# Optimization experiments

Hardware: AMD Instinct MI355X
Metric: run time of the kernel (lower is better)

## Reference

```python
import jax, jax.numpy as jnp
import numpy as np

B, C, H, W = 2, 256, 128, 128
NUM_CLASSES = 80
HIDDEN = 4
STRIDE = 8
NMS_CAND = 1000
IOU_THR = 0.65
MAX_DET = 100
PRIOR_BIAS = float(-np.log((1.0 - 0.01) / 0.01))  # RetinaNet-style prior prob bias


def _conv1x1(x, w, b):
    # x: [B,C,H,W], w: [O,C], b: [O]
    return jnp.einsum('bchw,oc->bohw', x, w) + b[None, :, None, None]


def _head(x, w_in, b_in, w_hid, b_hid, w_out, b_out):
    # ProjConv in-layer -> residual ProjConv hidden layers (kernel_size=1, skip=True) -> ProjConv out-layer
    x = _conv1x1(x, w_in, b_in)
    def step(h, wb):
        w, b = wb
        return h + _conv1x1(h, w, b), None
    x, _ = jax.lax.scan(step, x, (w_hid, b_hid))
    return _conv1x1(x, w_out, b_out)


def _nms_keep(boxes):
    # boxes: [K,4] in xyxy, pre-sorted by descending score
    x1, y1, x2, y2 = boxes[:, 0], boxes[:, 1], boxes[:, 2], boxes[:, 3]
    area = jnp.clip(x2 - x1, 0) * jnp.clip(y2 - y1, 0)
    lt = jnp.maximum(boxes[:, None, :2], boxes[None, :, :2])
    rb = jnp.minimum(boxes[:, None, 2:], boxes[None, :, 2:])
    wh = jnp.clip(rb - lt, 0)
    inter = wh[..., 0] * wh[..., 1]
    iou = inter / (area[:, None] + area[None, :] - inter + 1e-6)
    idx = jnp.arange(NMS_CAND)
    def body(i, keep):
        sup = (iou[i] > IOU_THR) & (idx > i) & keep[i]
        return keep & ~sup
    return jax.lax.fori_loop(0, NMS_CAND, body, jnp.ones((NMS_CAND,), bool))


def setup_inputs() -> dict:
    key = jax.random.key(0)
    ks = jax.random.split(key, 10)
    s = 0.02
    d = {'feat': jax.random.normal(ks[0], (B, C, H, W), jnp.float32)}
    d['cls_w_in'] = s * jax.random.normal(ks[1], (C, C), jnp.float32)
    d['cls_b_in'] = jnp.zeros((C,), jnp.float32)
    d['cls_w_hid'] = s * jax.random.normal(ks[2], (HIDDEN, C, C), jnp.float32)
    d['cls_b_hid'] = jnp.zeros((HIDDEN, C), jnp.float32)
    d['cls_w_out'] = s * jax.random.normal(ks[3], (NUM_CLASSES + 1, C), jnp.float32)
    d['cls_b_out'] = jnp.full((NUM_CLASSES + 1,), PRIOR_BIAS, jnp.float32)
    d['obj_w_in'] = s * jax.random.normal(ks[4], (C, C), jnp.float32)
    d['obj_b_in'] = jnp.zeros((C,), jnp.float32)
    d['obj_w_hid'] = s * jax.random.normal(ks[5], (HIDDEN, C, C), jnp.float32)
    d['obj_b_hid'] = jnp.zeros((HIDDEN, C), jnp.float32)
    d['obj_w_out'] = s * jax.random.normal(ks[6], (2, C), jnp.float32)
    d['obj_b_out'] = jnp.full((2,), PRIOR_BIAS, jnp.float32)
    d['box_w_in'] = s * jax.random.normal(ks[7], (C, C), jnp.float32)
    d['box_b_in'] = jnp.zeros((C,), jnp.float32)
    d['box_w_hid'] = s * jax.random.normal(ks[8], (HIDDEN, C, C), jnp.float32)
    d['box_b_hid'] = jnp.zeros((HIDDEN, C), jnp.float32)
    d['box_w_out'] = s * jax.random.normal(ks[9], (4, C), jnp.float32)
    d['box_b_out'] = jnp.zeros((4,), jnp.float32)
    return d


def reference(feat, cls_w_in, cls_b_in, cls_w_hid, cls_b_hid, cls_w_out, cls_b_out,
              obj_w_in, obj_b_in, obj_w_hid, obj_b_hid, obj_w_out, obj_b_out,
              box_w_in, box_b_in, box_w_hid, box_b_hid, box_w_out, box_b_out):
    cls_logits = _head(feat, cls_w_in, cls_b_in, cls_w_hid, cls_b_hid, cls_w_out, cls_b_out)
    obj_logits = _head(feat, obj_w_in, obj_b_in, obj_w_hid, obj_b_hid, obj_w_out, obj_b_out)
    box_logits = _head(feat, box_w_in, box_b_in, box_w_hid, box_b_hid, box_w_out, box_b_out)

    # per-location scores: class prob (excluding background channel) * objectness prob
    cls_prob = jax.nn.sigmoid(cls_logits[:, :NUM_CLASSES])        # [B,80,H,W]
    obj_prob = jax.nn.sigmoid(obj_logits[:, :1])                  # [B,1,H,W]
    sc = cls_prob * obj_prob
    score = sc.max(axis=1).reshape(B, -1)                         # [B,HW]
    label = sc.argmax(axis=1).reshape(B, -1)                      # [B,HW]

    # FCOS-style decode of (l,t,r,b) deltas around grid points
    xs = (jnp.arange(W, dtype=feat.dtype) + 0.5) * STRIDE
    ys = (jnp.arange(H, dtype=feat.dtype) + 0.5) * STRIDE
    px = jnp.broadcast_to(xs[None, :], (H, W)).reshape(-1)
    py = jnp.broadcast_to(ys[:, None], (H, W)).reshape(-1)
    ltrb = jnp.exp(box_logits).reshape(B, 4, -1) * STRIDE         # [B,4,HW]
    boxes = jnp.stack([px[None] - ltrb[:, 0], py[None] - ltrb[:, 1],
                       px[None] + ltrb[:, 2], py[None] + ltrb[:, 3]], axis=-1)  # [B,HW,4]

    # candidate selection + NMS + final top detections
    cand_sc, idx = jax.lax.top_k(score, NMS_CAND)                 # sorted descending
    cand_box = jnp.take_along_axis(boxes, idx[:, :, None], axis=1)
    cand_lab = jnp.take_along_axis(label, idx, axis=1)
    keep = jax.vmap(_nms_keep)(cand_box)                          # [B,K] bool
    det_sc, fin_idx = jax.lax.top_k(cand_sc * keep, MAX_DET)
    det_box = jnp.take_along_axis(cand_box, fin_idx[:, :, None], axis=1)
    det_lab = jnp.take_along_axis(cand_lab, fin_idx, axis=1)
    return det_box, det_sc, det_lab
```

## Files before the change

### kernel.cpp

```cpp
#include <hip/hip_runtime.h>
#include <math.h>

typedef unsigned int u32;
typedef unsigned long long u64;

#define HWSZ 16384
#define NCAND 1000
#define CAP 1024
#define NDET 100

__device__ __forceinline__ float sigmoidf_(float x) {
  return 1.0f / (1.0f + expf(-x));
}

template <int NROWS, bool FULLROWS>
__device__ __forceinline__ void run_gemm(const float* __restrict__ Wm,
                                         const float (*X)[128],
                                         float (*Wb)[2048], int tid, int rbase,
                                         int p0, float2 acc[16]) {
#pragma unroll
  for (int r = 0; r < 16; ++r) {
    acc[r].x = 0.f;
    acc[r].y = 0.f;
  }
  const int srow = tid >> 2;
  const int sq = (tid & 3) * 2;
  const bool sg = srow < NROWS;
  const bool cg = rbase < NROWS;

  if (sg) {
    float2 v = *(const float2*)(Wm + (size_t)srow * 256 + sq);
    *(float2*)&Wb[0][srow * 8 + sq] = v;
  }
  __syncthreads();

#pragma unroll 1
  for (int wn = 0; wn < 32; ++wn) {
    const int buf = wn & 1;
    float2 nv;
    const bool pre = sg && (wn + 1 < 32);
    if (pre)
      nv = *(const float2*)(Wm + (size_t)srow * 256 + (wn + 1) * 8 + sq);

    if (cg) {
#pragma unroll
      for (int j = 0; j < 2; ++j) {
        const int kb = wn * 2 + j;
        const float2 xv0 = *(const float2*)&X[kb * 4 + 0][p0];
        const float2 xv1 = *(const float2*)&X[kb * 4 + 1][p0];
        const float2 xv2 = *(const float2*)&X[kb * 4 + 2][p0];
        const float2 xv3 = *(const float2*)&X[kb * 4 + 3][p0];
#pragma unroll
        for (int r = 0; r < 16; ++r) {
          if (FULLROWS || rbase + r < NROWS) {
            const float4 wv =
                *(const float4*)&Wb[buf][(rbase + r) * 8 + j * 4];
            acc[r].x += wv.x * xv0.x;
            acc[r].y += wv.x * xv0.y;
            acc[r].x += wv.y * xv1.x;
            acc[r].y += wv.y * xv1.y;
            acc[r].x += wv.z * xv2.x;
            acc[r].y += wv.z * xv2.y;
            acc[r].x += wv.w * xv3.x;
            acc[r].y += wv.w * xv3.y;
          }
        }
      }
    }
    if (pre) *(float2*)&Wb[buf ^ 1][srow * 8 + sq] = nv;
    __syncthreads();
  }
}

__global__ __launch_bounds__(1024) void heads_fused(
    const float* __restrict__ feat, const float* __restrict__ ow_in,
    const float* __restrict__ ob_in, const float* __restrict__ ow_hid,
    const float* __restrict__ ob_hid, const float* __restrict__ ow_out,
    const float* __restrict__ ob_out, const float* __restrict__ cw_in,
    const float* __restrict__ cb_in, const float* __restrict__ cw_hid,
    const float* __restrict__ cb_hid, const float* __restrict__ cw_out,
    const float* __restrict__ cb_out, float* __restrict__ score,
    int* __restrict__ label) {
  __shared__ __align__(16) float X[256][128];
  __shared__ __align__(16) float Wb[2][2048];
  __shared__ float objL[128];
  __shared__ float smax[5][128];
  __shared__ int sarg[5][128];

  const int tid = threadIdx.x;
  const int wid = __builtin_amdgcn_readfirstlane(tid >> 6);
  const int ln = tid & 63;
  const int p0 = 2 * ln;
  const int rbase = wid * 16;
  const int batch = blockIdx.x >> 7;
  const int pbase = (blockIdx.x & 127) * 128;
  const float* fb = feat + (size_t)batch * 256 * HWSZ;

  for (int head = 0; head < 2; ++head) {
    const float* w_in = head ? cw_in : ow_in;
    const float* b_in = head ? cb_in : ob_in;
    const float* w_hid = head ? cw_hid : ow_hid;
    const float* b_hid = head ? cb_hid : ob_hid;

#pragma unroll
    for (int m = 0; m < 8; ++m) {
      int f4 = tid + 1024 * m;
      int c = f4 >> 5, col4 = (f4 & 31) * 4;
      *(float4*)&X[c][col4] =
          *(const float4*)(fb + (size_t)c * HWSZ + pbase + col4);
    }
    __syncthreads();

    float2 acc[16];
    for (int s = 0; s < 5; ++s) {
      const float* Wm = (s == 0) ? w_in : (w_hid + (size_t)(s - 1) * 65536);
      const float* bs = (s == 0) ? b_in : (b_hid + (s - 1) * 256);
      run_gemm<256, true>(Wm, X, Wb, tid, rbase, p0, acc);
#pragma unroll
      for (int r = 0; r < 16; ++r) {
        float b = bs[rbase + r];
        float2 v = make_float2(acc[r].x + b, acc[r].y + b);
        if (s > 0) {
          v.x += X[rbase + r][p0];
          v.y += X[rbase + r][p0 + 1];
        }
        *(float2*)&X[rbase + r][p0] = v;
      }
      __syncthreads();
    }

    if (head == 0) {
      run_gemm<2, false>(ow_out, X, Wb, tid, rbase, p0, acc);
      if (wid == 0) {
        float bo = ob_out[0];
        objL[p0] = sigmoidf_(acc[0].x + bo);
        objL[p0 + 1] = sigmoidf_(acc[0].y + bo);
      }
      __syncthreads();
    } else {
      run_gemm<80, true>(cw_out, X, Wb, tid, rbase, p0, acc);
      if (rbase < 80) {
        float ob0 = objL[p0], ob1 = objL[p0 + 1];
        float best0 = -1.f, best1 = -1.f;
        int a0 = 0, a1 = 0;
#pragma unroll
        for (int r = 0; r < 16; ++r) {
          float bb = cb_out[rbase + r];
          float s0 = sigmoidf_(acc[r].x + bb) * ob0;
          float s1 = sigmoidf_(acc[r].y + bb) * ob1;
          if (s0 > best0) {
            best0 = s0;
            a0 = rbase + r;
          }
          if (s1 > best1) {
            best1 = s1;
            a1 = rbase + r;
          }
        }
        smax[wid][p0] = best0;
        sarg[wid][p0] = a0;
        smax[wid][p0 + 1] = best1;
        sarg[wid][p0 + 1] = a1;
      }
      __syncthreads();
      if (tid < 128) {
        float best = -1.f;
        int ba = 0;
        for (int g = 0; g < 5; ++g) {
          float m = smax[g][tid];
          if (m > best) {
            best = m;
            ba = sarg[g][tid];
          }
        }
        score[batch * HWSZ + pbase + tid] = best;
        label[batch * HWSZ + pbase + tid] = ba;
      }
    }
  }
}

__global__ __launch_bounds__(1024) void box_all(
    const float* __restrict__ feat, const int* __restrict__ cand_idx,
    const float* __restrict__ w_in, const float* __restrict__ b_in,
    const float* __restrict__ w_hid, const float* __restrict__ b_hid,
    const float* __restrict__ w_out, const float* __restrict__ b_out,
    float* __restrict__ cand_box) {
  __shared__ float h[256][8];
  const int tid = threadIdx.x;
  const int batch = blockIdx.x >> 7;
  const int cbase = (blockIdx.x & 127) * 8;
  const float* fb = feat + (size_t)batch * 256 * HWSZ;

  for (int i = tid; i < 2048; i += 1024) {
    int k = i >> 3, c = i & 7;
    int r = cbase + c;
    float v = 0.f;
    if (r < NCAND) {
      int hw = cand_idx[batch * CAP + r];
      v = fb[(size_t)k * HWSZ + hw];
    }
    h[k][c] = v;
  }
  __syncthreads();

  const int wid = tid >> 6, ln = tid & 63;
  const int c = ln & 7, rr = ln >> 3;
  const int r0 = wid * 16 + rr, r1 = wid * 16 + 8 + rr;

  for (int s = 0; s < 5; ++s) {
    const float* Wm = (s == 0) ? w_in : (w_hid + (size_t)(s - 1) * 65536);
    const float* bs = (s == 0) ? b_in : (b_hid + (s - 1) * 256);
    float a0 = 0.f, a1 = 0.f;
    for (int kb = 0; kb < 64; ++kb) {
      float4 w0 = *(const float4*)&Wm[(size_t)r0 * 256 + kb * 4];
      float4 w1 = *(const float4*)&Wm[(size_t)r1 * 256 + kb * 4];
      float x0 = h[kb * 4 + 0][c], x1 = h[kb * 4 + 1][c];
      float x2 = h[kb * 4 + 2][c], x3 = h[kb * 4 + 3][c];
      a0 += w0.x * x0;
      a0 += w0.y * x1;
      a0 += w0.z * x2;
      a0 += w0.w * x3;
      a1 += w1.x * x0;
      a1 += w1.y * x1;
      a1 += w1.z * x2;
      a1 += w1.w * x3;
    }
    __syncthreads();
    float v0 = a0 + bs[r0], v1 = a1 + bs[r1];
    if (s > 0) {
      v0 += h[r0][c];
      v1 += h[r1][c];
    }
    h[r0][c] = v0;
    h[r1][c] = v1;
    __syncthreads();
  }

  if (tid < 32) {
    int row = tid >> 3, cc = tid & 7;
    int r = cbase + cc;
    if (r < NCAND) {
      float s = 0.f;
      for (int k = 0; k < 256; ++k) s += w_out[row * 256 + k] * h[k][cc];
      s += b_out[row];
      float e = expf(s) * 8.f;
      int hw = cand_idx[batch * CAP + r];
      int hh = hw >> 7, wwp = hw & 127;
      float px = (wwp + 0.5f) * 8.f, py = (hh + 0.5f) * 8.f;
      float coord = (row == 0)   ? px - e
                    : (row == 1) ? py - e
                    : (row == 2) ? px + e
                                 : py + e;
      cand_box[(size_t)(batch * CAP + r) * 4 + row] = coord;
    }
  }
}

__device__ __forceinline__ void suffix2048(u32* hist, int tid) {
  for (int d = 1; d < 2048; d <<= 1) {
    u32 v0 = hist[tid] + ((tid + d < 2048) ? hist[tid + d] : 0u);
    u32 v1 =
        hist[tid + 1024] + ((tid + 1024 + d < 2048) ? hist[tid + 1024 + d] : 0u);
    __syncthreads();
    hist[tid] = v0;
    hist[tid + 1024] = v1;
    __syncthreads();
  }
}

__global__ __launch_bounds__(1024) void topk_kernel(
    const float* __restrict__ score, const int* __restrict__ label,
    float* __restrict__ cand_sc, int* __restrict__ cand_idx,
    int* __restrict__ cand_lab) {
  __shared__ u32 hist[2048];
  __shared__ u64 buf[CAP];
  __shared__ u32 tiebuf[2048];
  __shared__ int sres[2];
  __shared__ int cA, cT;
  const int tid = threadIdx.x;
  const int b = blockIdx.x;
  const int base = b * HWSZ;
  u32 bits[16];
#pragma unroll
  for (int m = 0; m < 16; ++m)
    bits[m] = __float_as_uint(score[base + tid + 1024 * m]);

  int K = NCAND;
  u32 hi = 0;
  u32 thresh = 0;
  for (int lev = 0; lev < 3; ++lev) {
    hist[tid] = 0;
    hist[tid + 1024] = 0;
    __syncthreads();
#pragma unroll
    for (int m = 0; m < 16; ++m) {
      u32 v = bits[m];
      bool ok;
      int bin;
      if (lev == 0) {
        ok = true;
        bin = v >> 21;
      } else if (lev == 1) {
        ok = ((v >> 21) == hi);
        bin = (v >> 10) & 2047;
      } else {
        ok = ((v >> 10) == hi);
        bin = v & 1023;
      }
      if (ok) atomicAdd(&hist[bin], 1u);
    }
    __syncthreads();
    suffix2048(hist, tid);
#pragma unroll
    for (int e = 0; e < 2; ++e) {
      int i = tid + e * 1024;
      int Si = (int)hist[i];
      int Sn = (i + 1 < 2048) ? (int)hist[i + 1] : 0;
      if (Si >= K && Sn < K) {
        sres[0] = i;
        sres[1] = Sn;
      }
    }
    __syncthreads();
    int B = sres[0];
    K -= sres[1];
    if (lev == 0) hi = (u32)B;
    else if (lev == 1) hi = (hi << 11) | (u32)B;
    else thresh = (hi << 10) | (u32)B;
    __syncthreads();
  }
  const int T = K;

  if (tid == 0) {
    cA = 0;
    cT = 0;
  }
  __syncthreads();
#pragma unroll
  for (int m = 0; m < 16; ++m) {
    u32 v = bits[m];
    int idxp = tid + 1024 * m;
    if (v > thresh) {
      int pos = atomicAdd(&cA, 1);
      buf[pos] = ((u64)(~v) << 32) | (u32)idxp;
    } else if (v == thresh) {
      int pos = atomicAdd(&cT, 1);
      if (pos < 2048) tiebuf[pos] = (u32)idxp;
    }
  }
  __syncthreads();
  const int A = cA;
  int nT = cT < 2048 ? cT : 2048;
  for (int i = tid; i < 2048; i += 1024)
    if (i >= nT) tiebuf[i] = 0xFFFFFFFFu;
  __syncthreads();
  if (nT > 1) {
    for (int k = 2; k <= 2048; k <<= 1)
      for (int j = k >> 1; j > 0; j >>= 1) {
#pragma unroll
        for (int e = 0; e < 2; ++e) {
          int i = tid + e * 1024;
          int l = i ^ j;
          if (l > i) {
            u32 a = tiebuf[i], bb = tiebuf[l];
            bool up = ((i & k) == 0);
            if ((a > bb) == up) {
              tiebuf[i] = bb;
              tiebuf[l] = a;
            }
          }
        }
        __syncthreads();
      }
  }
  for (int t2 = tid; t2 < T; t2 += 1024)
    buf[A + t2] = ((u64)(~thresh) << 32) | tiebuf[t2];
  for (int i = tid; i < CAP; i += 1024)
    if (i >= NCAND) buf[i] = 0xFFFFFFFFFFFFFFFFull;
  __syncthreads();
  for (int k = 2; k <= 1024; k <<= 1)
    for (int j = k >> 1; j > 0; j >>= 1) {
      int i = tid, l = i ^ j;
      if (l > i) {
        u64 a = buf[i], bb = buf[l];
        bool up = ((i & k) == 0);
        if ((a > bb) == up) {
          buf[i] = bb;
          buf[l] = a;
        }
      }
      __syncthreads();
    }
  if (tid < NCAND) {
    u64 kv = buf[tid];
    u32 sb = ~(u32)(kv >> 32);
    int pix = (int)(kv & 0xFFFFFFFFull);
    cand_sc[b * CAP + tid] = __uint_as_float(sb);
    cand_idx[b * CAP + tid] = pix;
    cand_lab[b * CAP + tid] = label[base + pix];
  }
}

__global__ __launch_bounds__(1024) void nms_mask(
    const float* __restrict__ cand_box, u64* __restrict__ mask) {
  int bid = blockIdx.x;
  int b = bid / NCAND, i = bid % NCAND;
  int j = threadIdx.x;
  const float* bi = cand_box + (size_t)(b * CAP + i) * 4;
  float ix1 = bi[0], iy1 = bi[1], ix2 = bi[2], iy2 = bi[3];
  bool pred = false;
  if (j < NCAND && j > i) {
    const float* bj = cand_box + (size_t)(b * CAP + j) * 4;
    float jx1 = bj[0], jy1 = bj[1], jx2 = bj[2], jy2 = bj[3];
    float ai = fmaxf(ix2 - ix1, 0.f) * fmaxf(iy2 - iy1, 0.f);
    float aj = fmaxf(jx2 - jx1, 0.f) * fmaxf(jy2 - jy1, 0.f);
    float lx = fmaxf(ix1, jx1), ly = fmaxf(iy1, jy1);
    float rx = fminf(ix2, jx2), ry = fminf(iy2, jy2);
    float w = fmaxf(rx - lx, 0.f), h = fmaxf(ry - ly, 0.f);
    float inter = w * h;
    float iou = inter / (ai + aj - inter + 1e-6f);
    pred = iou > 0.65f;
  }
  u64 word = __ballot(pred);
  if ((j & 63) == 0) mask[(size_t)b * 16384 + i * 16 + (j >> 6)] = word;
}

__global__ void nms_finish(const u64* __restrict__ mask,
                           const float* __restrict__ cand_sc,
                           const int* __restrict__ cand_lab,
                           const float* __restrict__ cand_box,
                           float* __restrict__ out) {
  __shared__ u64 M[16000];
  int b = blockIdx.x, lane = threadIdx.x;
  for (int m = lane; m < 16000; m += 64) M[m] = mask[(size_t)b * 16384 + m];
  __syncthreads();
  u64 kw = 0ull;
  if (lane < 15) kw = ~0ull;
  else if (lane == 15) kw = (1ull << 40) - 1;
  for (int i = 0; i < NCAND; ++i) {
    u64 wi = __shfl(kw, i >> 6);
    if ((wi >> (i & 63)) & 1ull) {
      if (lane < 16) kw &= ~M[i * 16 + lane];
    }
  }
  u64 valid = 0ull;
  if (lane < 15) valid = ~0ull;
  else if (lane == 15) valid = (1ull << 40) - 1;
  kw &= valid;
  u64 sup = valid & ~kw;
  int ck = __popcll(kw), cs = __popcll(sup);
  int preK = 0, preS = 0, totK = 0;
  for (int q = 0; q < 16; ++q) {
    int vk = __shfl(ck, q), vs = __shfl(cs, q);
    if (q < lane) {
      preK += vk;
      preS += vs;
    }
    totK += vk;
  }
  float* obox = out;
  float* osc = out + 2 * NDET * 4;
  float* olab = out + 2 * NDET * 4 + 2 * NDET;
  if (lane < 16) {
    u64 m = kw;
    int pos = preK;
    while (m) {
      int bit = __ffsll((unsigned long long)m) - 1;
      m &= m - 1;
      int j = lane * 64 + bit;
      if (pos < NDET) {
        osc[b * NDET + pos] = cand_sc[b * CAP + j];
        olab[b * NDET + pos] = (float)cand_lab[b * CAP + j];
        const float* bx = cand_box + (size_t)(b * CAP + j) * 4;
        float* dst = obox + (size_t)(b * NDET + pos) * 4;
        dst[0] = bx[0];
        dst[1] = bx[1];
        dst[2] = bx[2];
        dst[3] = bx[3];
      }
      ++pos;
    }
    m = sup;
    pos = totK + preS;
    while (m) {
      int bit = __ffsll((unsigned long long)m) - 1;
      m &= m - 1;
      int j = lane * 64 + bit;
      if (pos < NDET) {
        osc[b * NDET + pos] = 0.0f;
        olab[b * NDET + pos] = (float)cand_lab[b * CAP + j];
        const float* bx = cand_box + (size_t)(b * CAP + j) * 4;
        float* dst = obox + (size_t)(b * NDET + pos) * 4;
        dst[0] = bx[0];
        dst[1] = bx[1];
        dst[2] = bx[2];
        dst[3] = bx[3];
      }
      ++pos;
    }
  }
}

extern "C" void kernel_launch(void* const* d_in, const int* in_sizes, int n_in,
                              void* d_out, int out_size, void* d_ws,
                              size_t ws_size, hipStream_t stream) {
  (void)in_sizes;
  (void)n_in;
  (void)out_size;
  (void)ws_size;
  const float* feat = (const float*)d_in[0];
  const float* cls_w_in = (const float*)d_in[1];
  const float* cls_b_in = (const float*)d_in[2];
  const float* cls_w_hid = (const float*)d_in[3];
  const float* cls_b_hid = (const float*)d_in[4];
  const float* cls_w_out = (const float*)d_in[5];
  const float* cls_b_out = (const float*)d_in[6];
  const float* obj_w_in = (const float*)d_in[7];
  const float* obj_b_in = (const float*)d_in[8];
  const float* obj_w_hid = (const float*)d_in[9];
  const float* obj_b_hid = (const float*)d_in[10];
  const float* obj_w_out = (const float*)d_in[11];
  const float* obj_b_out = (const float*)d_in[12];
  const float* box_w_in = (const float*)d_in[13];
  const float* box_b_in = (const float*)d_in[14];
  const float* box_w_hid = (const float*)d_in[15];
  const float* box_b_hid = (const float*)d_in[16];
  const float* box_w_out = (const float*)d_in[17];
  const float* box_b_out = (const float*)d_in[18];
  float* out = (float*)d_out;

  char* w = (char*)d_ws;
  float* scoreArr = (float*)w;
  int* labelArr = (int*)(w + 131072);
  float* cand_sc = (float*)(w + 262144);
  int* cand_idx = (int*)(w + 270336);
  int* cand_lab = (int*)(w + 278528);
  float* cand_box = (float*)(w + 286720);
  u64* maskArr = (u64*)(w + 319488);

  heads_fused<<<256, 1024, 0, stream>>>(
      feat, obj_w_in, obj_b_in, obj_w_hid, obj_b_hid, obj_w_out, obj_b_out,
      cls_w_in, cls_b_in, cls_w_hid, cls_b_hid, cls_w_out, cls_b_out, scoreArr,
      labelArr);
  topk_kernel<<<2, 1024, 0, stream>>>(scoreArr, labelArr, cand_sc, cand_idx,
                                      cand_lab);
  box_all<<<256, 1024, 0, stream>>>(feat, cand_idx, box_w_in, box_b_in,
                                    box_w_hid, box_b_hid, box_w_out, box_b_out,
                                    cand_box);
  nms_mask<<<2000, 1024, 0, stream>>>(cand_box, maskArr);
  nms_finish<<<2, 64, 0, stream>>>(maskArr, cand_sc, cand_lab, cand_box, out);
}
```

Baseline: 926.5 us.

## Halve heads_fused pixel tile to 64 and double the grid to 512 blocks

Result: slower. 1.490 ms (+60.9%).

```diff
diff --git a/kernel.cpp b/kernel.cpp
--- a/kernel.cpp
+++ b/kernel.cpp
@@ -14,60 +14,44 @@
 }
 
 template <int NROWS, bool FULLROWS>
-__device__ __forceinline__ void run_gemm(const float* __restrict__ Wm,
-                                         const float (*X)[128],
-                                         float (*Wb)[2048], int tid, int rbase,
-                                         int p0, float2 acc[16]) {
-#pragma unroll
-  for (int r = 0; r < 16; ++r) {
-    acc[r].x = 0.f;
-    acc[r].y = 0.f;
-  }
+__device__ __forceinline__ void run_gemm64(const float* __restrict__ Wm,
+                                           const float (*X)[64],
+                                           float (*Wb)[1024], int tid,
+                                           int rbase, int ln, float acc[16]) {
+#pragma unroll
+  for (int r = 0; r < 16; ++r) acc[r] = 0.f;
   const int srow = tid >> 2;
-  const int sq = (tid & 3) * 2;
+  const int sq = tid & 3;
   const bool sg = srow < NROWS;
   const bool cg = rbase < NROWS;
 
-  if (sg) {
-    float2 v = *(const float2*)(Wm + (size_t)srow * 256 + sq);
-    *(float2*)&Wb[0][srow * 8 + sq] = v;
-  }
+  if (sg) Wb[0][srow * 4 + sq] = Wm[(size_t)srow * 256 + sq];
   __syncthreads();
 
 #pragma unroll 1
-  for (int wn = 0; wn < 32; ++wn) {
+  for (int wn = 0; wn < 64; ++wn) {
     const int buf = wn & 1;
-    float2 nv;
-    const bool pre = sg && (wn + 1 < 32);
-    if (pre)
-      nv = *(const float2*)(Wm + (size_t)srow * 256 + (wn + 1) * 8 + sq);
+    float nv;
+    const bool pre = sg && (wn + 1 < 64);
+    if (pre) nv = Wm[(size_t)srow * 256 + (wn + 1) * 4 + sq];
 
     if (cg) {
-#pragma unroll
-      for (int j = 0; j < 2; ++j) {
-        const int kb = wn * 2 + j;
-        const float2 xv0 = *(const float2*)&X[kb * 4 + 0][p0];
-        const float2 xv1 = *(const float2*)&X[kb * 4 + 1][p0];
-        const float2 xv2 = *(const float2*)&X[kb * 4 + 2][p0];
-        const float2 xv3 = *(const float2*)&X[kb * 4 + 3][p0];
-#pragma unroll
-        for (int r = 0; r < 16; ++r) {
-          if (FULLROWS || rbase + r < NROWS) {
-            const float4 wv =
-                *(const float4*)&Wb[buf][(rbase + r) * 8 + j * 4];
-            acc[r].x += wv.x * xv0.x;
-            acc[r].y += wv.x * xv0.y;
-            acc[r].x += wv.y * xv1.x;
-            acc[r].y += wv.y * xv1.y;
-            acc[r].x += wv.z * xv2.x;
-            acc[r].y += wv.z * xv2.y;
-            acc[r].x += wv.w * xv3.x;
-            acc[r].y += wv.w * xv3.y;
-          }
+      const float xv0 = X[wn * 4 + 0][ln];
+      const float xv1 = X[wn * 4 + 1][ln];
+      const float xv2 = X[wn * 4 + 2][ln];
+      const float xv3 = X[wn * 4 + 3][ln];
+#pragma unroll
+      for (int r = 0; r < 16; ++r) {
+        if (FULLROWS || rbase + r < NROWS) {
+          const float4 wv = *(const float4*)&Wb[buf][(rbase + r) * 4];
+          acc[r] += wv.x * xv0;
+          acc[r] += wv.y * xv1;
+          acc[r] += wv.z * xv2;
+          acc[r] += wv.w * xv3;
         }
       }
     }
-    if (pre) *(float2*)&Wb[buf ^ 1][srow * 8 + sq] = nv;
+    if (pre) Wb[buf ^ 1][srow * 4 + sq] = nv;
     __syncthreads();
   }
 }
@@ -81,20 +65,21 @@
     const float* __restrict__ cb_hid, const float* __restrict__ cw_out,
     const float* __restrict__ cb_out, float* __restrict__ score,
     int* __restrict__ label) {
-  __shared__ __align__(16) float X[256][128];
-  __shared__ __align__(16) float Wb[2][2048];
-  __shared__ float objL[128];
-  __shared__ float smax[5][128];
-  __shared__ int sarg[5][128];
+  __shared__ __align__(16) float X[256][64];
+  __shared__ __align__(16) float Wb[2][1024];
+  __shared__ float objL[64];
+  __shared__ float smax[5][64];
+  __shared__ int sarg[5][64];
 
   const int tid = threadIdx.x;
   const int wid = __builtin_amdgcn_readfirstlane(tid >> 6);
   const int ln = tid & 63;
-  const int p0 = 2 * ln;
   const int rbase = wid * 16;
-  const int batch = blockIdx.x >> 7;
-  const int pbase = (blockIdx.x & 127) * 128;
+  const int batch = blockIdx.x >> 8;
+  const int pbase = (blockIdx.x & 255) * 64;
   const float* fb = feat + (size_t)batch * 256 * HWSZ;
+
+  float acc[16];
 
   for (int head = 0; head < 2; ++head) {
     const float* w_in = head ? cw_in : ow_in;
@@ -103,67 +88,52 @@
     const float* b_hid = head ? cb_hid : ob_hid;
 
 #pragma unroll
-    for (int m = 0; m < 8; ++m) {
+    for (int m = 0; m < 4; ++m) {
       int f4 = tid + 1024 * m;
-      int c = f4 >> 5, col4 = (f4 & 31) * 4;
+      int c = f4 >> 4, col4 = (f4 & 15) * 4;
       *(float4*)&X[c][col4] =
           *(const float4*)(fb + (size_t)c * HWSZ + pbase + col4);
     }
     __syncthreads();
 
-    float2 acc[16];
     for (int s = 0; s < 5; ++s) {
       const float* Wm = (s == 0) ? w_in : (w_hid + (size_t)(s - 1) * 65536);
       const float* bs = (s == 0) ? b_in : (b_hid + (s - 1) * 256);
-      run_gemm<256, true>(Wm, X, Wb, tid, rbase, p0, acc);
+      run_gemm64<256, true>(Wm, X, Wb, tid, rbase, ln, acc);
 #pragma unroll
       for (int r = 0; r < 16; ++r) {
-        float b = bs[rbase + r];
-        float2 v = make_float2(acc[r].x + b, acc[r].y + b);
-        if (s > 0) {
-          v.x += X[rbase + r][p0];
-          v.y += X[rbase + r][p0 + 1];
-        }
-        *(float2*)&X[rbase + r][p0] = v;
+        float v = acc[r] + bs[rbase + r];
+        if (s > 0) v += X[rbase + r][ln];
+        X[rbase + r][ln] = v;
       }
       __syncthreads();
     }
 
     if (head == 0) {
-      run_gemm<2, false>(ow_out, X, Wb, tid, rbase, p0, acc);
+      run_gemm64<2, false>(ow_out, X, Wb, tid, rbase, ln, acc);
       if (wid == 0) {
-        float bo = ob_out[0];
-        objL[p0] = sigmoidf_(acc[0].x + bo);
-        objL[p0 + 1] = sigmoidf_(acc[0].y + bo);
+        objL[ln] = sigmoidf_(acc[0] + ob_out[0]);
       }
       __syncthreads();
     } else {
-      run_gemm<80, true>(cw_out, X, Wb, tid, rbase, p0, acc);
+      run_gemm64<80, true>(cw_out, X, Wb, tid, rbase, ln, acc);
       if (rbase < 80) {
-        float ob0 = objL[p0], ob1 = objL[p0 + 1];
-        float best0 = -1.f, best1 = -1.f;
-        int a0 = 0, a1 = 0;
+        float ob = objL[ln];
+        float best = -1.f;
+        int ba = 0;
 #pragma unroll
         for (int r = 0; r < 16; ++r) {
-          float bb = cb_out[rbase + r];
-          float s0 = sigmoidf_(acc[r].x + bb) * ob0;
-          float s1 = sigmoidf_(acc[r].y + bb) * ob1;
-          if (s0 > best0) {
-            best0 = s0;
-            a0 = rbase + r;
-          }
-          if (s1 > best1) {
-            best1 = s1;
-            a1 = rbase + r;
+          float s0 = sigmoidf_(acc[r] + cb_out[rbase + r]) * ob;
+          if (s0 > best) {
+            best = s0;
+            ba = rbase + r;
           }
         }
-        smax[wid][p0] = best0;
-        sarg[wid][p0] = a0;
-        smax[wid][p0 + 1] = best1;
-        sarg[wid][p0 + 1] = a1;
+        smax[wid][ln] = best;
+        sarg[wid][ln] = ba;
       }
       __syncthreads();
-      if (tid < 128) {
+      if (tid < 64) {
         float best = -1.f;
         int ba = 0;
         for (int g = 0; g < 5; ++g) {
@@ -539,7 +509,7 @@
   float* cand_box = (float*)(w + 286720);
   u64* maskArr = (u64*)(w + 319488);
 
-  heads_fused<<<256, 1024, 0, stream>>>(
+  heads_fused<<<512, 1024, 0, stream>>>(
       feat, obj_w_in, obj_b_in, obj_w_hid, obj_b_hid, obj_w_out, obj_b_out,
       cls_w_in, cls_b_in, cls_w_hid, cls_b_hid, cls_w_out, cls_b_out, scoreArr,
       labelArr);
```
